# Optimization experiments

Measured on AMD Instinct MI355X. Metric: run time of the kernel, lower is better.

The kernel has to match this reference:

```python
import jax, jax.numpy as jnp
import numpy as np
import math

HIDDEN = 1024
HEADS = 16
HEAD_DIM = HIDDEN // HEADS


def setup_inputs() -> dict:
    key = jax.random.key(0)
    ks = jax.random.split(key, 7)
    B, S = 2, 2048
    scale = 1.0 / math.sqrt(HIDDEN)
    return {
        "x": jax.random.normal(ks[0], (B, S, HIDDEN), dtype=jnp.float32),
        "Wq": jax.random.normal(ks[1], (HIDDEN, HIDDEN), dtype=jnp.float32) * scale,
        "Wk": jax.random.normal(ks[2], (HIDDEN, HIDDEN), dtype=jnp.float32) * scale,
        "Wv": jax.random.normal(ks[3], (HIDDEN, HIDDEN), dtype=jnp.float32) * scale,
        "Wo": jax.random.normal(ks[4], (HIDDEN, HIDDEN), dtype=jnp.float32) * scale,
        "quantum_phase": jax.random.normal(ks[5], (HEADS, HEAD_DIM), dtype=jnp.float32),
        "quantum_amplitude": jnp.ones((HEADS, HEAD_DIM), dtype=jnp.float32),
    }


def reference(x, Wq, Wk, Wv, Wo, quantum_phase, quantum_amplitude):
    B, S, d = x.shape
    H, D = HEADS, HEAD_DIM

    # per-head/per-channel quantum modulation: real(x*exp(i*phase)) == x*cos(phase)
    mod = (jnp.cos(quantum_phase) * quantum_amplitude)[None, :, None, :]  # [1,H,1,D]

    def proj(W):
        return (x @ W).reshape(B, S, H, D).transpose(0, 2, 1, 3)  # [B,H,S,D]

    q = proj(Wq) * mod
    k = proj(Wk) * mod
    v = proj(Wv) * mod

    scores = jnp.einsum("bhid,bhjd->bhij", q, k) / math.sqrt(D)  # [B,H,S,S]

    # quantum interference: scores[i,j] *= cos(2*pi*(i-j)/S)
    idx = jnp.arange(S, dtype=jnp.float32)
    cos_mat = jnp.cos(2.0 * math.pi * (idx[:, None] - idx[None, :]) / S)  # [S,S]
    scores = scores * cos_mat

    w = jax.nn.softmax(scores, axis=-1)
    # superposition of attention weights with key-rolled copy
    w = (w + jnp.roll(w, 1, axis=-1)) / math.sqrt(2.0)

    out = jnp.einsum("bhij,bhjd->bhid", w, v)  # [B,H,S,D]
    out = out.transpose(0, 2, 1, 3).reshape(B, S, d)
    return out @ Wo
```

## Files before the change

### kernel.cpp

```cpp
#include <hip/hip_runtime.h>
#include <hip/hip_bf16.h>
#include <math.h>

#define HIDDEN 1024
#define HEADS  16
#define HDIM   64
#define BATCH  2
#define SEQ    2048
#define ROWS   (BATCH*SEQ)
#define BH     (BATCH*HEADS)

typedef __attribute__((ext_vector_type(8))) short  short8;
typedef __attribute__((ext_vector_type(8))) __bf16 bf16x8;
typedef __attribute__((ext_vector_type(4))) float  f32x4;

static __device__ __forceinline__ unsigned short f2bf(float f) {
    unsigned int u = __builtin_bit_cast(unsigned int, f);
    u += 0x7FFFu + ((u >> 16) & 1u);
    return (unsigned short)(u >> 16);
}
static __device__ __forceinline__ float bf2f(unsigned short h) {
    unsigned int u = ((unsigned int)h) << 16;
    return __builtin_bit_cast(float, u);
}
static __device__ __forceinline__ f32x4 mfma16(short8 a, short8 b, f32x4 c) {
    return __builtin_amdgcn_mfma_f32_16x16x32_bf16(
        __builtin_bit_cast(bf16x8, a), __builtin_bit_cast(bf16x8, b), c, 0, 0, 0);
}
static __device__ __forceinline__ void gl_lds16(const unsigned short* g, unsigned short* l) {
    __builtin_amdgcn_global_load_lds(
        (const __attribute__((address_space(1))) unsigned int*)g,
        (__attribute__((address_space(3))) unsigned int*)l, 16, 0, 0);
}

__global__ __launch_bounds__(256) void prep_kernel(
    const float* __restrict__ x, unsigned short* __restrict__ xb,
    const float* __restrict__ w0, const float* __restrict__ w1,
    const float* __restrict__ w2, const float* __restrict__ w3,
    unsigned short* __restrict__ wt,
    const float* __restrict__ qp, const float* __restrict__ qa,
    float* __restrict__ mod, float* __restrict__ mod2,
    float* __restrict__ posc, float* __restrict__ poss) {
    __shared__ unsigned short tile[64][72];
    const int bid = blockIdx.x;
    const int t = threadIdx.x;
    if (bid < 4096) {
        int i = (bid * 256 + t) * 4;
        float4 v = *(const float4*)(x + i);
        ushort4 o;
        o.x = f2bf(v.x); o.y = f2bf(v.y); o.z = f2bf(v.z); o.w = f2bf(v.w);
        *(ushort4*)(xb + i) = o;
        if (bid < 8) {
            int k = bid * 256 + t;
            if (k < HIDDEN) {
                float m = cosf(qp[k]) * qa[k];
                mod[k] = m;
                mod2[k] = m * m * 0.18033688011112042f;
            }
            if (k < SEQ) {
                float ang = (float)k * (6.283185307179586f / (float)SEQ);
                posc[k] = cosf(ang);
                poss[k] = sinf(ang);
            }
        }
        return;
    }
    int rem = bid - 4096;
    int z = rem >> 8, r2 = rem & 255;
    int n0 = (r2 & 15) * 64, k0 = (r2 >> 4) * 64;
    const float* src = (z == 0) ? w0 : (z == 1) ? w1 : (z == 2) ? w2 : w3;
    unsigned short* dst = wt + (size_t)z * HIDDEN * HIDDEN;
    int cg = t & 15, r0 = t >> 4;
#pragma unroll
    for (int rr = 0; rr < 4; rr++) {
        int kl = r0 + rr * 16;
        float4 v = *(const float4*)(src + (size_t)(k0 + kl) * HIDDEN + n0 + cg * 4);
        tile[cg*4+0][kl] = f2bf(v.x);
        tile[cg*4+1][kl] = f2bf(v.y);
        tile[cg*4+2][kl] = f2bf(v.z);
        tile[cg*4+3][kl] = f2bf(v.w);
    }
    __syncthreads();
#pragma unroll
    for (int rr = 0; rr < 4; rr++) {
        int nl = r0 + rr * 16;
        ushort4 o;
        o.x = tile[nl][cg*4+0]; o.y = tile[nl][cg*4+1];
        o.z = tile[nl][cg*4+2]; o.w = tile[nl][cg*4+3];
        *(ushort4*)(dst + (size_t)(n0 + nl) * HIDDEN + k0 + cg * 4) = o;
    }
}

__global__ __launch_bounds__(256) void gemm_kernel(
    const unsigned short* __restrict__ A, const unsigned short* __restrict__ WtBase,
    unsigned short* __restrict__ CBase, const float* __restrict__ mod) {
    __shared__ unsigned short Alds[128 * 64];
    __shared__ unsigned short Blds[64 * 64];
    const int mode = blockIdx.z;
    const unsigned short* Bt = WtBase + (size_t)mode * HIDDEN * HIDDEN;
    unsigned short* Cout = CBase + (size_t)mode * ROWS * HIDDEN;
    const int m0 = blockIdx.x * 128, n0 = blockIdx.y * 64;
    const int tid = threadIdx.x;
    const int wave = tid >> 6, lane = tid & 63, quad = lane >> 4, l15 = lane & 15;
    const int wr = wave >> 1, wc = wave & 1;
    const int srow = lane >> 3;
    const int schunk = (lane & 7) ^ (srow & 7);

    f32x4 acc[4][2];
    const f32x4 z4 = {0.f, 0.f, 0.f, 0.f};
#pragma unroll
    for (int i = 0; i < 4; i++)
#pragma unroll
        for (int j = 0; j < 2; j++) acc[i][j] = z4;

    for (int k0 = 0; k0 < HIDDEN; k0 += 64) {
#pragma unroll
        for (int p = 0; p < 4; p++) {
            int rbase = p * 32 + wave * 8;
            gl_lds16(A + (size_t)(m0 + rbase + srow) * HIDDEN + k0 + schunk * 8,
                     &Alds[rbase * 64]);
        }
#pragma unroll
        for (int p = 0; p < 2; p++) {
            int rbase = p * 32 + wave * 8;
            gl_lds16(Bt + (size_t)(n0 + rbase + srow) * HIDDEN + k0 + schunk * 8,
                     &Blds[rbase * 64]);
        }
        __syncthreads();
        short8 aF[4][2], bF[2][2];
#pragma unroll
        for (int h = 0; h < 2; h++) {
#pragma unroll
            for (int i = 0; i < 4; i++) {
                int row = wr * 64 + i * 16 + l15;
                aF[i][h] = *(const short8*)(&Alds[row * 64 + ((h * 4 + quad) ^ (l15 & 7)) * 8]);
            }
#pragma unroll
            for (int j = 0; j < 2; j++) {
                int row = wc * 32 + j * 16 + l15;
                bF[j][h] = *(const short8*)(&Blds[row * 64 + ((h * 4 + quad) ^ (l15 & 7)) * 8]);
            }
        }
#pragma unroll
        for (int h = 0; h < 2; h++)
#pragma unroll
            for (int i = 0; i < 4; i++)
#pragma unroll
                for (int j = 0; j < 2; j++)
                    acc[i][j] = mfma16(aF[i][h], bF[j][h], acc[i][j]);
        __syncthreads();
    }

#pragma unroll
    for (int i = 0; i < 4; i++) {
        int mbase = m0 + wr * 64 + i * 16 + quad * 4;
#pragma unroll
        for (int j = 0; j < 2; j++) {
            int n = n0 + wc * 32 + j * 16 + l15;
            float vm = (mode == 2) ? mod[n] : 1.0f;
#pragma unroll
            for (int r = 0; r < 4; r++) {
                int mm = mbase + r;
                Cout[(size_t)mm * HIDDEN + n] = f2bf(acc[i][j][r] * vm);
            }
        }
    }
}

__global__ __launch_bounds__(256) void gemm_o_kernel(
    const unsigned short* __restrict__ A, const unsigned short* __restrict__ Bt,
    float* __restrict__ Out) {
    __shared__ unsigned short Alds[128 * 64];
    __shared__ unsigned short Blds[64 * 64];
    const int m0 = blockIdx.x * 128, n0 = blockIdx.y * 64;
    const int tid = threadIdx.x;
    const int wave = tid >> 6, lane = tid & 63, quad = lane >> 4, l15 = lane & 15;
    const int wr = wave >> 1, wc = wave & 1;
    const int srow = lane >> 3;
    const int schunk = (lane & 7) ^ (srow & 7);

    f32x4 acc[4][2];
    const f32x4 z4 = {0.f, 0.f, 0.f, 0.f};
#pragma unroll
    for (int i = 0; i < 4; i++)
#pragma unroll
        for (int j = 0; j < 2; j++) acc[i][j] = z4;

    for (int k0 = 0; k0 < HIDDEN; k0 += 64) {
#pragma unroll
        for (int p = 0; p < 4; p++) {
            int rbase = p * 32 + wave * 8;
            gl_lds16(A + (size_t)(m0 + rbase + srow) * HIDDEN + k0 + schunk * 8,
                     &Alds[rbase * 64]);
        }
#pragma unroll
        for (int p = 0; p < 2; p++) {
            int rbase = p * 32 + wave * 8;
            gl_lds16(Bt + (size_t)(n0 + rbase + srow) * HIDDEN + k0 + schunk * 8,
                     &Blds[rbase * 64]);
        }
        __syncthreads();
        short8 aF[4][2], bF[2][2];
#pragma unroll
        for (int h = 0; h < 2; h++) {
#pragma unroll
            for (int i = 0; i < 4; i++) {
                int row = wr * 64 + i * 16 + l15;
                aF[i][h] = *(const short8*)(&Alds[row * 64 + ((h * 4 + quad) ^ (l15 & 7)) * 8]);
            }
#pragma unroll
            for (int j = 0; j < 2; j++) {
                int row = wc * 32 + j * 16 + l15;
                bF[j][h] = *(const short8*)(&Blds[row * 64 + ((h * 4 + quad) ^ (l15 & 7)) * 8]);
            }
        }
#pragma unroll
        for (int h = 0; h < 2; h++)
#pragma unroll
            for (int i = 0; i < 4; i++)
#pragma unroll
                for (int j = 0; j < 2; j++)
                    acc[i][j] = mfma16(aF[i][h], bF[j][h], acc[i][j]);
        __syncthreads();
    }

#pragma unroll
    for (int i = 0; i < 4; i++) {
        int mbase = m0 + wr * 64 + i * 16 + quad * 4;
#pragma unroll
        for (int j = 0; j < 2; j++) {
            int n = n0 + wc * 32 + j * 16 + l15;
#pragma unroll
            for (int r = 0; r < 4; r++)
                Out[(size_t)(mbase + r) * HIDDEN + n] = acc[i][j][r];
        }
    }
}

__global__ __launch_bounds__(256) void vshift_kernel(const unsigned short* __restrict__ Vm,
                                                     unsigned short* __restrict__ Vpt) {
    __shared__ unsigned short lds[65][72];
    int bh = blockIdx.x, b = bh >> 4, h = bh & 15;
    int s0 = blockIdx.y * 64;
    int t = threadIdx.x;
    int cg = t & 15, r0 = t >> 4;
#pragma unroll
    for (int rr = 0; rr < 4; rr++) {
        int row = r0 + rr * 16;
        ushort4 v = *(const ushort4*)(Vm + ((size_t)(b * SEQ + s0 + row)) * HIDDEN + h * 64 + cg * 4);
        *(ushort4*)(&lds[row][cg * 4]) = v;
    }
    if (t < 16) {
        int srow = (s0 + 64) & (SEQ - 1);
        ushort4 v = *(const ushort4*)(Vm + ((size_t)(b * SEQ + srow)) * HIDDEN + h * 64 + t * 4);
        *(ushort4*)(&lds[64][t * 4]) = v;
    }
    __syncthreads();
    int d = t & 63, sb = (t >> 6) * 16;
    unsigned short outv[16];
#pragma unroll
    for (int k = 0; k < 16; k++) {
        float a = bf2f(lds[sb + k][d]), bb = bf2f(lds[sb + k + 1][d]);
        outv[k] = f2bf((a + bb) * 0.7071067811865476f);
    }
    unsigned short* dst = Vpt + ((size_t)bh * 64 + d) * SEQ + s0 + sb;
#pragma unroll
    for (int k = 0; k < 16; k += 4) {
        ushort4 o; o.x = outv[k]; o.y = outv[k+1]; o.z = outv[k+2]; o.w = outv[k+3];
        *(ushort4*)(dst + k) = o;
    }
}

#define KT 128
#define PSTR2 44
__global__ __launch_bounds__(256) void attn_kernel(const unsigned short* __restrict__ Cq,
                                                   const unsigned short* __restrict__ Ck,
                                                   const unsigned short* __restrict__ Vpt,
                                                   unsigned short* __restrict__ Ob,
                                                   const float* __restrict__ mod2,
                                                   const float* __restrict__ posc,
                                                   const float* __restrict__ poss) {
    __shared__ unsigned short Klds[2][KT * 64];
    __shared__ unsigned short Vtlds[2][64 * 128];
    __shared__ unsigned short Plds[4 * 32 * PSTR2];
    const int bh = blockIdx.x;
    const int b = bh >> 4, h = bh & 15;
    const int tid = threadIdx.x, wave = tid >> 6, lane = tid & 63;
    const int quad = lane >> 4, l15 = lane & 15;
    const int q0 = blockIdx.y * 128 + wave * 32;

    short8 qf[2][2];
#pragma unroll
    for (int g = 0; g < 2; g++) {
        int ss = q0 + g * 16 + l15;
        const unsigned short* crow = Cq + ((size_t)(b * SEQ + ss)) * HIDDEN + h * 64;
#pragma unroll
        for (int kk = 0; kk < 2; kk++) {
            int bd = kk * 32 + quad * 8;
            short8 u = *(const short8*)(crow + bd);
            short8 q;
#pragma unroll
            for (int e = 0; e < 8; e++)
                q[e] = (short)f2bf(bf2f((unsigned short)u[e]) * mod2[h * 64 + bd + e]);
            qf[g][kk] = q;
        }
    }
    float ci[2][4], si[2][4];
#pragma unroll
    for (int g = 0; g < 2; g++)
#pragma unroll
        for (int r = 0; r < 4; r++) {
            int ss = q0 + g * 16 + quad * 4 + r;
            ci[g][r] = posc[ss];
            si[g][r] = poss[ss];
        }

    short8 ones;
#pragma unroll
    for (int e = 0; e < 8; e++) ones[e] = (short)0x3F80;

    const f32x4 z4 = {0.f, 0.f, 0.f, 0.f};
    f32x4 acc[2][4], accden[2];
#pragma unroll
    for (int g = 0; g < 2; g++) {
#pragma unroll
        for (int dt = 0; dt < 4; dt++) acc[g][dt] = z4;
        accden[g] = z4;
    }

    unsigned short* pw = &Plds[wave * 32 * PSTR2];

    const unsigned short* Kbh = Ck  + ((size_t)b * SEQ) * HIDDEN + h * 64;
    const unsigned short* Vbh = Vpt + (size_t)bh * 64 * SEQ;

    auto stage = [&](int j, int buf) {
#pragma unroll
        for (int p = 0; p < 4; p++) {
            int rb = p * 32 + wave * 8;
            int r  = rb + (lane >> 3);
            int c  = (lane & 7) ^ (r & 7);
            gl_lds16(Kbh + (size_t)(j + r) * HIDDEN + c * 8, &Klds[buf][rb * 64]);
        }
#pragma unroll
        for (int p = 0; p < 4; p++) {
            int rb = p * 16 + wave * 4;
            int r  = rb + (lane >> 4);
            int c  = (lane & 15) ^ (r & 15);
            gl_lds16(Vbh + (size_t)r * SEQ + j + c * 8, &Vtlds[buf][rb * 128]);
        }
    };

    float cjc[8], sjc[8];
#pragma unroll
    for (int tt = 0; tt < 8; tt++) {
        int jj = tt * 16 + l15;
        cjc[tt] = posc[jj]; sjc[tt] = poss[jj];
    }

    stage(0, 0);
    const int NIT = SEQ / KT;
    for (int it = 0; it < NIT; it++) {
        __syncthreads();
        float cjn[8], sjn[8];
        if (it + 1 < NIT) {
            stage((it + 1) * KT, (it + 1) & 1);
#pragma unroll
            for (int tt = 0; tt < 8; tt++) {
                int jj = (it + 1) * KT + tt * 16 + l15;
                cjn[tt] = posc[jj]; sjn[tt] = poss[jj];
            }
        } else {
#pragma unroll
            for (int tt = 0; tt < 8; tt++) { cjn[tt] = 0.f; sjn[tt] = 0.f; }
        }
        const int buf = it & 1;

#pragma unroll
        for (int chunk = 0; chunk < 4; chunk++) {
#pragma unroll
            for (int t2i = 0; t2i < 2; t2i++) {
                int tt = chunk * 2 + t2i;
                float cj = cjc[tt], sj = sjc[tt];
                f32x4 sc[2] = {z4, z4};
#pragma unroll
                for (int kk = 0; kk < 2; kk++) {
                    int ch = (kk * 4 + quad) ^ (l15 & 7);
                    short8 kf = *(const short8*)(&Klds[buf][(tt * 16 + l15) * 64 + ch * 8]);
#pragma unroll
                    for (int g = 0; g < 2; g++)
                        sc[g] = mfma16(qf[g][kk], kf, sc[g]);
                }
#pragma unroll
                for (int g = 0; g < 2; g++) {
#pragma unroll
                    for (int r = 0; r < 4; r++) {
                        float w = ci[g][r] * cj + si[g][r] * sj;
                        float p = __builtin_amdgcn_exp2f(sc[g][r] * w);
                        unsigned short pt = (unsigned short)(__builtin_bit_cast(unsigned int, p) >> 16);
                        pw[(g * 16 + quad * 4 + r) * PSTR2 + t2i * 16 + l15] = pt;
                    }
                }
            }
            short8 pa0 = *(const short8*)(&pw[(l15) * PSTR2 + quad * 8]);
            short8 pa1 = *(const short8*)(&pw[(16 + l15) * PSTR2 + quad * 8]);
            accden[0] = mfma16(pa0, ones, accden[0]);
            accden[1] = mfma16(pa1, ones, accden[1]);
#pragma unroll
            for (int dt = 0; dt < 4; dt++) {
                int ch = (chunk * 4 + quad) ^ l15;
                short8 vb = *(const short8*)(&Vtlds[buf][(dt * 16 + l15) * 128 + ch * 8]);
                acc[0][dt] = mfma16(pa0, vb, acc[0][dt]);
                acc[1][dt] = mfma16(pa1, vb, acc[1][dt]);
            }
        }
#pragma unroll
        for (int tt = 0; tt < 8; tt++) { cjc[tt] = cjn[tt]; sjc[tt] = sjn[tt]; }
    }

#pragma unroll
    for (int g = 0; g < 2; g++) {
        float rinv[4];
#pragma unroll
        for (int r = 0; r < 4; r++) rinv[r] = 1.0f / accden[g][r];
#pragma unroll
        for (int dt = 0; dt < 4; dt++) {
#pragma unroll
            for (int r = 0; r < 4; r++) {
                int q = q0 + g * 16 + quad * 4 + r;
                int d = dt * 16 + l15;
                Ob[((size_t)(b * SEQ + q)) * HIDDEN + h * 64 + d] = f2bf(acc[g][dt][r] * rinv[r]);
            }
        }
    }
}

extern "C" void kernel_launch(void* const* d_in, const int* in_sizes, int n_in,
                              void* d_out, int out_size, void* d_ws, size_t ws_size,
                              hipStream_t stream) {
    const float* x  = (const float*)d_in[0];
    const float* Wq = (const float*)d_in[1];
    const float* Wk = (const float*)d_in[2];
    const float* Wv = (const float*)d_in[3];
    const float* Wo = (const float*)d_in[4];
    const float* qp = (const float*)d_in[5];
    const float* qa = (const float*)d_in[6];
    char* ws = (char*)d_ws;

    unsigned short* Xb  = (unsigned short*)(ws);
    unsigned short* Wt  = (unsigned short*)(ws + (size_t)( 8 << 20));
    unsigned short* Cq  = (unsigned short*)(ws + (size_t)(16 << 20));
    unsigned short* Ck  = (unsigned short*)(ws + (size_t)(24 << 20));
    unsigned short* Cv  = (unsigned short*)(ws + (size_t)(32 << 20));
    unsigned short* Vpt = (unsigned short*)(ws + (size_t)(40 << 20));
    float* mod  = (float*)(ws + (size_t)(48 << 20));
    float* mod2 = mod + 1024;
    float* posc = mod2 + 1024;
    float* poss = posc + 2048;
    float* out  = (float*)d_out;

    prep_kernel<<<5120, 256, 0, stream>>>(x, Xb, Wq, Wk, Wv, Wo, Wt,
                                          qp, qa, mod, mod2, posc, poss);
    gemm_kernel<<<dim3(32, 16, 3), 256, 0, stream>>>(Xb, Wt, Cq, mod);
    vshift_kernel<<<dim3(32, 32), 256, 0, stream>>>(Cv, Vpt);
    attn_kernel<<<dim3(32, 16), 256, 0, stream>>>(Cq, Ck, Vpt, Xb , mod2, posc, poss);
    gemm_o_kernel<<<dim3(32, 16), 256, 0, stream>>>(Xb, Wt + (size_t)3 * HIDDEN * HIDDEN, out);
}
```

Before: 225.1 us.

## Keep attention probabilities in registers via transposed QK MFMA and permlane swaps

The QK^T MFMA now takes its operands in swapped order, so each lane holds scores along keys for one query. Probabilities are packed to bf16 with v_cvt_pk_bf16_f32 and rearranged with permlane32/permlane16 swaps into the A-operand layout for the PV MFMA. This removes the per-wave LDS staging buffer for P and its write/read round trip. The position cos/sin values are now loaded as vectors per chunk instead of being prefetched into registers, and s_setprio brackets are added around the MFMA sections. The risk is that the permlane layout must match the MFMA operand layout exactly for results to stay correct.

```diff
diff --git a/kernel.cpp b/kernel.cpp
--- a/kernel.cpp
+++ b/kernel.cpp
@@ -13,6 +13,7 @@
 typedef __attribute__((ext_vector_type(8))) short  short8;
 typedef __attribute__((ext_vector_type(8))) __bf16 bf16x8;
 typedef __attribute__((ext_vector_type(4))) float  f32x4;
+typedef __attribute__((ext_vector_type(4))) unsigned int uint4v;
 
 static __device__ __forceinline__ unsigned short f2bf(float f) {
     unsigned int u = __builtin_bit_cast(unsigned int, f);
@@ -272,7 +273,6 @@
 }
 
 #define KT 128
-#define PSTR2 44
 __global__ __launch_bounds__(256) void attn_kernel(const unsigned short* __restrict__ Cq,
                                                    const unsigned short* __restrict__ Ck,
                                                    const unsigned short* __restrict__ Vpt,
@@ -282,7 +282,6 @@
                                                    const float* __restrict__ poss) {
     __shared__ unsigned short Klds[2][KT * 64];
     __shared__ unsigned short Vtlds[2][64 * 128];
-    __shared__ unsigned short Plds[4 * 32 * PSTR2];
     const int bh = blockIdx.x;
     const int b = bh >> 4, h = bh & 15;
     const int tid = threadIdx.x, wave = tid >> 6, lane = tid & 63;
@@ -305,15 +304,12 @@
             qf[g][kk] = q;
         }
     }
-    float ci[2][4], si[2][4];
-#pragma unroll
-    for (int g = 0; g < 2; g++)
-#pragma unroll
-        for (int r = 0; r < 4; r++) {
-            int ss = q0 + g * 16 + quad * 4 + r;
-            ci[g][r] = posc[ss];
-            si[g][r] = poss[ss];
-        }
+    float ci_[2], si_[2];
+#pragma unroll
+    for (int g = 0; g < 2; g++) {
+        ci_[g] = posc[q0 + g * 16 + l15];
+        si_[g] = poss[q0 + g * 16 + l15];
+    }
 
     short8 ones;
 #pragma unroll
@@ -327,8 +323,6 @@
         for (int dt = 0; dt < 4; dt++) acc[g][dt] = z4;
         accden[g] = z4;
     }
-
-    unsigned short* pw = &Plds[wave * 32 * PSTR2];
 
     const unsigned short* Kbh = Ck  + ((size_t)b * SEQ) * HIDDEN + h * 64;
     const unsigned short* Vbh = Vpt + (size_t)bh * 64 * SEQ;
@@ -350,71 +344,75 @@
         }
     };
 
-    float cjc[8], sjc[8];
-#pragma unroll
-    for (int tt = 0; tt < 8; tt++) {
-        int jj = tt * 16 + l15;
-        cjc[tt] = posc[jj]; sjc[tt] = poss[jj];
-    }
-
     stage(0, 0);
     const int NIT = SEQ / KT;
     for (int it = 0; it < NIT; it++) {
         __syncthreads();
-        float cjn[8], sjn[8];
-        if (it + 1 < NIT) {
-            stage((it + 1) * KT, (it + 1) & 1);
-#pragma unroll
-            for (int tt = 0; tt < 8; tt++) {
-                int jj = (it + 1) * KT + tt * 16 + l15;
-                cjn[tt] = posc[jj]; sjn[tt] = poss[jj];
-            }
-        } else {
-#pragma unroll
-            for (int tt = 0; tt < 8; tt++) { cjn[tt] = 0.f; sjn[tt] = 0.f; }
-        }
+        if (it + 1 < NIT) stage((it + 1) * KT, (it + 1) & 1);
         const int buf = it & 1;
 
 #pragma unroll
         for (int chunk = 0; chunk < 4; chunk++) {
+            const int jb = it * KT + chunk * 32 + quad * 4;
+            f32x4 cjA[2], sjA[2];
+            cjA[0] = *(const f32x4*)(posc + jb);
+            sjA[0] = *(const f32x4*)(poss + jb);
+            cjA[1] = *(const f32x4*)(posc + jb + 16);
+            sjA[1] = *(const f32x4*)(poss + jb + 16);
+
+            f32x4 sc[2][2];
+            sc[0][0] = z4; sc[0][1] = z4; sc[1][0] = z4; sc[1][1] = z4;
+            __builtin_amdgcn_s_setprio(1);
 #pragma unroll
             for (int t2i = 0; t2i < 2; t2i++) {
                 int tt = chunk * 2 + t2i;
-                float cj = cjc[tt], sj = sjc[tt];
-                f32x4 sc[2] = {z4, z4};
 #pragma unroll
                 for (int kk = 0; kk < 2; kk++) {
                     int ch = (kk * 4 + quad) ^ (l15 & 7);
                     short8 kf = *(const short8*)(&Klds[buf][(tt * 16 + l15) * 64 + ch * 8]);
-#pragma unroll
-                    for (int g = 0; g < 2; g++)
-                        sc[g] = mfma16(qf[g][kk], kf, sc[g]);
+                    sc[0][t2i] = mfma16(kf, qf[0][kk], sc[0][t2i]);
+                    sc[1][t2i] = mfma16(kf, qf[1][kk], sc[1][t2i]);
                 }
-#pragma unroll
-                for (int g = 0; g < 2; g++) {
-#pragma unroll
-                    for (int r = 0; r < 4; r++) {
-                        float w = ci[g][r] * cj + si[g][r] * sj;
-                        float p = __builtin_amdgcn_exp2f(sc[g][r] * w);
-                        unsigned short pt = (unsigned short)(__builtin_bit_cast(unsigned int, p) >> 16);
-                        pw[(g * 16 + quad * 4 + r) * PSTR2 + t2i * 16 + l15] = pt;
+            }
+            __builtin_amdgcn_s_setprio(0);
+
+            short8 pa[2];
+#pragma unroll
+            for (int g = 0; g < 2; g++) {
+                unsigned int w_[4];
+#pragma unroll
+                for (int t2i = 0; t2i < 2; t2i++) {
+#pragma unroll
+                    for (int hp = 0; hp < 2; hp++) {
+                        float wl = ci_[g] * cjA[t2i][2 * hp]     + si_[g] * sjA[t2i][2 * hp];
+                        float wh = ci_[g] * cjA[t2i][2 * hp + 1] + si_[g] * sjA[t2i][2 * hp + 1];
+                        float pl = __builtin_amdgcn_exp2f(sc[g][t2i][2 * hp]     * wl);
+                        float ph = __builtin_amdgcn_exp2f(sc[g][t2i][2 * hp + 1] * wh);
+                        unsigned int w;
+                        asm("v_cvt_pk_bf16_f32 %0, %1, %2" : "=v"(w) : "v"(pl), "v"(ph));
+                        w_[t2i * 2 + hp] = w;
                     }
                 }
-            }
-            short8 pa0 = *(const short8*)(&pw[(l15) * PSTR2 + quad * 8]);
-            short8 pa1 = *(const short8*)(&pw[(16 + l15) * PSTR2 + quad * 8]);
-            accden[0] = mfma16(pa0, ones, accden[0]);
-            accden[1] = mfma16(pa1, ones, accden[1]);
+                auto t02 = __builtin_amdgcn_permlane32_swap(w_[0], w_[2], false, false);
+                auto a02 = __builtin_amdgcn_permlane16_swap(t02[0], t02[1], false, false);
+                auto t13 = __builtin_amdgcn_permlane32_swap(w_[1], w_[3], false, false);
+                auto a13 = __builtin_amdgcn_permlane16_swap(t13[0], t13[1], false, false);
+                uint4v pword;
+                pword[0] = a02[0]; pword[1] = a13[0]; pword[2] = a02[1]; pword[3] = a13[1];
+                pa[g] = __builtin_bit_cast(short8, pword);
+                accden[g] = mfma16(pa[g], ones, accden[g]);
+            }
+
+            __builtin_amdgcn_s_setprio(1);
 #pragma unroll
             for (int dt = 0; dt < 4; dt++) {
                 int ch = (chunk * 4 + quad) ^ l15;
                 short8 vb = *(const short8*)(&Vtlds[buf][(dt * 16 + l15) * 128 + ch * 8]);
-                acc[0][dt] = mfma16(pa0, vb, acc[0][dt]);
-                acc[1][dt] = mfma16(pa1, vb, acc[1][dt]);
-            }
-        }
-#pragma unroll
-        for (int tt = 0; tt < 8; tt++) { cjc[tt] = cjn[tt]; sjc[tt] = sjn[tt]; }
+                acc[0][dt] = mfma16(pa[0], vb, acc[0][dt]);
+                acc[1][dt] = mfma16(pa[1], vb, acc[1][dt]);
+            }
+            __builtin_amdgcn_s_setprio(0);
+        }
     }
 
 #pragma unroll
```

Result: faster. 216.9 us (-3.7%).
